# Performance work log

Hardware: AMD Instinct MI355X
Metric: run time of the kernel (lower is better)

The kernel has to match this reference:

```python
import jax, jax.numpy as jnp
import numpy as np

N_NODES = 50000
N_EDGES = 800000
IN_FEAT = 8
H = 128
L = 6
NUM_GRAPHS = 64
EPS_MSG = 1e-7
EPS_SM = 1e-16
LN_EPS = 1e-5


def _ln(x, g, b):
    mu = jnp.mean(x, axis=-1, keepdims=True)
    var = jnp.var(x, axis=-1, keepdims=True)
    return (x - mu) * jax.lax.rsqrt(var + LN_EPS) * g + b


def setup_inputs() -> dict:
    key = jax.random.key(0)
    ks = jax.random.split(key, 12)
    x = jax.random.normal(ks[0], (N_NODES, IN_FEAT), dtype=jnp.float32)
    edge_index = jax.random.randint(ks[1], (2, N_EDGES), 0, N_NODES)
    batch_ids = jnp.sort(jax.random.randint(ks[2], (N_NODES,), 0, NUM_GRAPHS))
    s = 0.05
    return {
        "x": x,
        "edge_index": edge_index,
        "batch_ids": batch_ids,
        "node_W": jax.random.normal(ks[3], (IN_FEAT, H), jnp.float32) * s,
        "node_b": jnp.zeros((H,), jnp.float32),
        "ln_g": jnp.ones((L, H), jnp.float32),
        "ln_b": jnp.zeros((L, H), jnp.float32),
        "t": jnp.ones((L,), jnp.float32),
        "W1": jax.random.normal(ks[4], (L, H, 2 * H), jnp.float32) * s,
        "b1": jnp.zeros((L, 2 * H), jnp.float32),
        "mln_g": jnp.ones((L, 2 * H), jnp.float32),
        "mln_b": jnp.zeros((L, 2 * H), jnp.float32),
        "W2": jax.random.normal(ks[5], (L, 2 * H, H), jnp.float32) * s,
        "b2": jnp.zeros((L, H), jnp.float32),
    }


def reference(x, edge_index, batch_ids, node_W, node_b, ln_g, ln_b, t, W1, b1, mln_g, mln_b, W2, b2):
    src, dst = edge_index[0], edge_index[1]
    n = x.shape[0]
    # node encoder
    x = x @ node_W + node_b  # [N, H]
    for i in range(L):
        # DeepGCNLayer res+: h = relu(LN(x)); x = x + conv(h)
        h = jax.nn.relu(_ln(x, ln_g[i], ln_b[i]))
        # GENConv message: relu(x_j) + eps
        m = jax.nn.relu(h[src]) + EPS_MSG  # [E, H]
        # softmax aggregation over destination segments (temperature t)
        scaled = m * t[i]
        mx = jax.ops.segment_max(scaled, dst, num_segments=n)
        mx = jnp.where(jnp.isfinite(mx), mx, 0.0)
        e = jnp.exp(scaled - mx[dst])
        denom = jax.ops.segment_sum(e, dst, num_segments=n)
        aggr = jax.ops.segment_sum(m * e, dst, num_segments=n) / (denom + EPS_SM)
        # GENConv: out = mlp(aggr + x_r)
        u = aggr + h
        u = u @ W1[i] + b1[i]
        u = jax.nn.relu(_ln(u, mln_g[i], mln_b[i]))
        u = u @ W2[i] + b2[i]
        x = x + u
    # global_add_pool
    return jax.ops.segment_sum(x, batch_ids, num_segments=NUM_GRAPHS)  # [G, H]
```

## Files before the change

### kernel.cpp

```cpp
#include <hip/hip_runtime.h>
#include <hip/hip_bf16.h>
#include <math.h>

#define N_NODES 50000
#define N_EDGES 800000
#define IN_FEAT 8
#define HDIM 128
#define NLAYERS 6
#define NUM_GRAPHS 64
#define EPS_MSG 1e-7f
#define EPS_SM 1e-16f
#define LN_EPS 1e-5f
#define SCAN_NB 49

typedef __attribute__((ext_vector_type(8))) short short8;
typedef __attribute__((ext_vector_type(4))) float floatx4;

__device__ __forceinline__ ushort f2bf(float x) {
    __hip_bfloat16 h = __float2bfloat16(x);
    return *reinterpret_cast<ushort*>(&h);
}
__device__ __forceinline__ float bf2f(ushort u) {
    unsigned int v = ((unsigned int)u) << 16;
    return __uint_as_float(v);
}

__global__ void k_encode_ln(const float* __restrict__ xin, const float* __restrict__ W,
                            const float* __restrict__ bias, const float* __restrict__ g0,
                            const float* __restrict__ b0, float* __restrict__ X,
                            ushort2* __restrict__ Hb) {
    __shared__ float sW[IN_FEAT * HDIM];
    int tid = threadIdx.x;
    int wid = tid >> 6, lane = tid & 63;
    for (int i = tid; i < IN_FEAT * HDIM; i += 256) sW[i] = W[i];
    __syncthreads();
    int n = blockIdx.x * 4 + wid;
    if (n >= N_NODES) return;
    int c0 = 2 * lane, c1 = 2 * lane + 1;
    float a0 = bias[c0], a1 = bias[c1];
#pragma unroll
    for (int f = 0; f < IN_FEAT; ++f) {
        float xf = xin[n * IN_FEAT + f];
        a0 += xf * sW[f * HDIM + c0];
        a1 += xf * sW[f * HDIM + c1];
    }
    float2 xv; xv.x = a0; xv.y = a1;
    *(float2*)(X + (size_t)n * HDIM + c0) = xv;
    float s = a0 + a1, sq = a0 * a0 + a1 * a1;
#pragma unroll
    for (int off = 32; off; off >>= 1) {
        s += __shfl_xor(s, off, 64);
        sq += __shfl_xor(sq, off, 64);
    }
    float mean = s * (1.f / 128.f);
    float var = sq * (1.f / 128.f) - mean * mean;
    float inv = rsqrtf(var + LN_EPS);
    float h0 = (a0 - mean) * inv * g0[c0] + b0[c0];
    float h1 = (a1 - mean) * inv * g0[c1] + b0[c1];
    ushort2 o;
    o.x = f2bf(fmaxf(h0, 0.f));
    o.y = f2bf(fmaxf(h1, 0.f));
    Hb[(size_t)n * 64 + lane] = o;
}

__global__ void k_hist(const int* __restrict__ dst, int* __restrict__ deg) {
    int i = blockIdx.x * blockDim.x + threadIdx.x;
    if (i < N_EDGES) atomicAdd(&deg[dst[i]], 1);
}

__global__ void k_bsum(const int* __restrict__ deg, int* __restrict__ bsum) {
    int i = blockIdx.x * 1024 + threadIdx.x;
    int v = (i < N_NODES) ? deg[i] : 0;
#pragma unroll
    for (int off = 32; off; off >>= 1) v += __shfl_xor(v, off, 64);
    __shared__ int wsum[16];
    int wid = threadIdx.x >> 6;
    if ((threadIdx.x & 63) == 0) wsum[wid] = v;
    __syncthreads();
    if (threadIdx.x < 16) {
        int s = wsum[threadIdx.x];
#pragma unroll
        for (int off = 8; off; off >>= 1) s += __shfl_xor(s, off, 16);
        if (threadIdx.x == 0) bsum[blockIdx.x] = s;
    }
}

__global__ void k_scan_small(int* __restrict__ bsum) {
    int lane = threadIdx.x;
    int orig = (lane < SCAN_NB) ? bsum[lane] : 0;
    int v = orig;
#pragma unroll
    for (int off = 1; off < 64; off <<= 1) {
        int u = __shfl_up(v, off, 64);
        if (lane >= off) v += u;
    }
    if (lane < SCAN_NB) bsum[lane] = v - orig;
}

__global__ void k_scan_final(const int* __restrict__ deg, const int* __restrict__ bsum,
                             int* __restrict__ row_ptr, int* __restrict__ cursor) {
    __shared__ int wsum[16];
    int i = blockIdx.x * 1024 + threadIdx.x;
    int t = threadIdx.x;
    int lane = t & 63, wid = t >> 6;
    int orig = (i < N_NODES) ? deg[i] : 0;
    int v = orig;
#pragma unroll
    for (int off = 1; off < 64; off <<= 1) {
        int u = __shfl_up(v, off, 64);
        if (lane >= off) v += u;
    }
    if (lane == 63) wsum[wid] = v;
    __syncthreads();
    if (t < 16) {
        int s = wsum[t];
#pragma unroll
        for (int off = 1; off < 16; off <<= 1) {
            int u = __shfl_up(s, off, 16);
            if (t >= off) s += u;
        }
        wsum[t] = s;
    }
    __syncthreads();
    int base = bsum[blockIdx.x] + (wid ? wsum[wid - 1] : 0);
    int excl = base + v - orig;
    if (i < N_NODES) {
        row_ptr[i] = excl;
        cursor[i] = excl;
    }
    if (i == 0) row_ptr[N_NODES] = N_EDGES;
}

__global__ void k_scatter(const int* __restrict__ src, const int* __restrict__ dst,
                          int* __restrict__ cursor, int* __restrict__ csr_src) {
    int i = blockIdx.x * blockDim.x + threadIdx.x;
    if (i < N_EDGES) {
        int pos = atomicAdd(&cursor[dst[i]], 1);
        csr_src[pos] = src[i];
    }
}

__global__ void k_prep(const float* __restrict__ W1, const float* __restrict__ W2,
                       ushort* __restrict__ Wp1, ushort* __restrict__ Wp2) {
    int idx = blockIdx.x * 256 + threadIdx.x;
    if (idx < 24576) {
        int lane = idx & 63;
        int frag = idx >> 6;
        int cf = frag & 15, kb = (frag >> 4) & 3, l = frag >> 6;
        const float* Wl = W1 + (size_t)l * 128 * 256;
        ushort* o = Wp1 + (size_t)idx * 8;
        int k0 = kb * 32 + (lane >> 4) * 8;
        int c = cf * 16 + (lane & 15);
#pragma unroll
        for (int j = 0; j < 8; ++j) o[j] = f2bf(Wl[(k0 + j) * 256 + c]);
    } else if (idx < 49152) {
        int i2 = idx - 24576;
        int lane = i2 & 63;
        int frag = i2 >> 6;
        int cf = frag & 7, kb = (frag >> 3) & 7, l = frag >> 6;
        const float* Wl = W2 + (size_t)l * 256 * 128;
        ushort* o = Wp2 + (size_t)i2 * 8;
        int k0 = kb * 32 + (lane >> 4) * 8;
        int c = cf * 16 + (lane & 15);
#pragma unroll
        for (int j = 0; j < 8; ++j) o[j] = f2bf(Wl[(k0 + j) * 128 + c]);
    }
}

__global__ __launch_bounds__(256) void k_aggr(const ushort2* __restrict__ Hh,
                                              const int* __restrict__ row_ptr,
                                              const int* __restrict__ csr,
                                              const float* __restrict__ t_all,
                                              int layer, ushort2* __restrict__ U) {
    __shared__ float part[2][64][4];
    int tid = threadIdx.x;
    int wid = tid >> 6, lane = tid & 63;
    int local = wid >> 1;
    int half = wid & 1;
    int n = blockIdx.x * 2 + local;
    float tt = t_all[layer];
    int beg = row_ptr[n], end = row_ptr[n + 1];
    int cnt = end - beg;
    int mycnt = (cnt - half + 1) >> 1;
    float den0 = 0.f, den1 = 0.f, num0 = 0.f, num1 = 0.f;
    unsigned laneoff = (unsigned)(lane << 2);

    auto proc = [&](ushort2 c) {
        float m0 = bf2f(c.x) + EPS_MSG;
        float m1 = bf2f(c.y) + EPS_MSG;
        float e0 = __expf(m0 * tt);
        float e1 = __expf(m1 * tt);
        den0 += e0; num0 += m0 * e0;
        den1 += e1; num1 += m1 * e1;
    };
    auto LDI = [&](int k) -> ushort2 {
        int kk = (k < mycnt) ? k : mycnt - 1;
        int sidx = csr[beg + half + 2 * kk];
        return *(const ushort2*)((const char*)Hh + (((unsigned)sidx << 8) + laneoff));
    };

    if (mycnt > 0) {
        ushort2 p0 = LDI(0), p1 = LDI(1), p2 = LDI(2), p3 = LDI(3),
                p4 = LDI(4), p5 = LDI(5), p6 = LDI(6), p7 = LDI(7);
        int e = 0;
        while (e + 8 <= mycnt) {
            ushort2 c0 = p0, c1 = p1, c2 = p2, c3 = p3,
                    c4 = p4, c5 = p5, c6 = p6, c7 = p7;
            p0 = LDI(e + 8);  p1 = LDI(e + 9);  p2 = LDI(e + 10); p3 = LDI(e + 11);
            p4 = LDI(e + 12); p5 = LDI(e + 13); p6 = LDI(e + 14); p7 = LDI(e + 15);
            proc(c0); proc(c1); proc(c2); proc(c3);
            proc(c4); proc(c5); proc(c6); proc(c7);
            e += 8;
        }
        int rem = mycnt - e;
        if (rem > 0) proc(p0);
        if (rem > 1) proc(p1);
        if (rem > 2) proc(p2);
        if (rem > 3) proc(p3);
        if (rem > 4) proc(p4);
        if (rem > 5) proc(p5);
        if (rem > 6) proc(p6);
    }

    if (half == 1) {
        part[local][lane][0] = num0;
        part[local][lane][1] = num1;
        part[local][lane][2] = den0;
        part[local][lane][3] = den1;
    }
    __syncthreads();
    if (half == 0) {
        num0 += part[local][lane][0];
        num1 += part[local][lane][1];
        den0 += part[local][lane][2];
        den1 += part[local][lane][3];
        float a0 = num0 / (den0 + EPS_SM);
        float a1 = num1 / (den1 + EPS_SM);
        ushort2 hs = Hh[(size_t)n * 64 + lane];
        ushort2 o;
        o.x = f2bf(a0 + bf2f(hs.x));
        o.y = f2bf(a1 + bf2f(hs.y));
        U[(size_t)n * 64 + lane] = o;
    }
}

__global__ __launch_bounds__(256) void k_mlp_fused(
    const ushort* __restrict__ U, float* __restrict__ X,
    const short8* __restrict__ Wp1, const short8* __restrict__ Wp2,
    const float* __restrict__ b1, const float* __restrict__ mg,
    const float* __restrict__ mb, const float* __restrict__ b2,
    const float* __restrict__ nlg, const float* __restrict__ nlb,
    ushort* __restrict__ HbOut, int writeHb) {
    __shared__ ushort sBuf[64 * 264];
    __shared__ float sStat[4][64][2];
    __shared__ float sMV[64][2];
    int tid = threadIdx.x;
    int w = tid >> 6, lane = tid & 63;
    int g = lane >> 4, c15 = lane & 15;
    int n0 = blockIdx.x * 64;

#pragma unroll
    for (int i = 0; i < 4; ++i) {
        int id = tid + i * 256;
        int row = id >> 4, cc = id & 15;
        int n = n0 + row;
        short8 v = {0, 0, 0, 0, 0, 0, 0, 0};
        if (n < N_NODES) v = *(const short8*)(U + (size_t)n * 128 + cc * 8);
        *(short8*)(sBuf + row * 136 + cc * 8) = v;
    }
    __syncthreads();

    floatx4 acc1[4][4];
#pragma unroll
    for (int rf = 0; rf < 4; ++rf)
#pragma unroll
        for (int cf = 0; cf < 4; ++cf) acc1[rf][cf] = (floatx4){0.f, 0.f, 0.f, 0.f};

#pragma unroll
    for (int kb = 0; kb < 4; ++kb) {
        short8 bfr[4];
#pragma unroll
        for (int cf = 0; cf < 4; ++cf) bfr[cf] = Wp1[(kb * 16 + w * 4 + cf) * 64 + lane];
        short8 af[4];
#pragma unroll
        for (int rf = 0; rf < 4; ++rf)
            af[rf] = *(const short8*)(sBuf + (rf * 16 + c15) * 136 + kb * 32 + g * 8);
#pragma unroll
        for (int rf = 0; rf < 4; ++rf)
#pragma unroll
            for (int cf = 0; cf < 4; ++cf)
                acc1[rf][cf] = __builtin_amdgcn_mfma_f32_16x16x32_bf16(af[rf], bfr[cf], acc1[rf][cf], 0, 0, 0);
    }

    int colb = w * 64;
    float bv[4], gv[4], bbv[4];
#pragma unroll
    for (int cf = 0; cf < 4; ++cf) {
        int c = colb + cf * 16 + c15;
        bv[cf] = b1[c]; gv[cf] = mg[c]; bbv[cf] = mb[c];
    }
    float sS[4][4], sQ[4][4];
#pragma unroll
    for (int rf = 0; rf < 4; ++rf)
#pragma unroll
        for (int reg = 0; reg < 4; ++reg) {
            float s = 0.f, q = 0.f;
#pragma unroll
            for (int cf = 0; cf < 4; ++cf) {
                float v = acc1[rf][cf][reg] + bv[cf];
                acc1[rf][cf][reg] = v;
                s += v; q += v * v;
            }
            sS[rf][reg] = s; sQ[rf][reg] = q;
        }
#pragma unroll
    for (int off = 1; off < 16; off <<= 1)
#pragma unroll
        for (int rf = 0; rf < 4; ++rf)
#pragma unroll
            for (int reg = 0; reg < 4; ++reg) {
                sS[rf][reg] += __shfl_xor(sS[rf][reg], off, 64);
                sQ[rf][reg] += __shfl_xor(sQ[rf][reg], off, 64);
            }
    if (c15 == 0) {
#pragma unroll
        for (int rf = 0; rf < 4; ++rf)
#pragma unroll
            for (int reg = 0; reg < 4; ++reg) {
                int row = rf * 16 + g * 4 + reg;
                sStat[w][row][0] = sS[rf][reg];
                sStat[w][row][1] = sQ[rf][reg];
            }
    }
    __syncthreads();
    if (tid < 64) {
        float s = sStat[0][tid][0] + sStat[1][tid][0] + sStat[2][tid][0] + sStat[3][tid][0];
        float q = sStat[0][tid][1] + sStat[1][tid][1] + sStat[2][tid][1] + sStat[3][tid][1];
        float mean = s * (1.f / 256.f);
        float var = q * (1.f / 256.f) - mean * mean;
        sMV[tid][0] = mean;
        sMV[tid][1] = rsqrtf(var + LN_EPS);
    }
    __syncthreads();

#pragma unroll
    for (int rf = 0; rf < 4; ++rf)
#pragma unroll
        for (int reg = 0; reg < 4; ++reg) {
            int row = rf * 16 + g * 4 + reg;
            float mean = sMV[row][0], inv = sMV[row][1];
#pragma unroll
            for (int cf = 0; cf < 4; ++cf) {
                float v = (acc1[rf][cf][reg] - mean) * inv * gv[cf] + bbv[cf];
                sBuf[row * 264 + colb + cf * 16 + c15] = f2bf(fmaxf(v, 0.f));
            }
        }
    __syncthreads();

    floatx4 acc2[4][2];
#pragma unroll
    for (int rf = 0; rf < 4; ++rf) {
        acc2[rf][0] = (floatx4){0.f, 0.f, 0.f, 0.f};
        acc2[rf][1] = (floatx4){0.f, 0.f, 0.f, 0.f};
    }
#pragma unroll
    for (int kb = 0; kb < 8; ++kb) {
        short8 bfr[2];
#pragma unroll
        for (int cf = 0; cf < 2; ++cf) bfr[cf] = Wp2[(kb * 8 + w * 2 + cf) * 64 + lane];
        short8 af[4];
#pragma unroll
        for (int rf = 0; rf < 4; ++rf)
            af[rf] = *(const short8*)(sBuf + (rf * 16 + c15) * 264 + kb * 32 + g * 8);
#pragma unroll
        for (int rf = 0; rf < 4; ++rf)
#pragma unroll
            for (int cf = 0; cf < 2; ++cf)
                acc2[rf][cf] = __builtin_amdgcn_mfma_f32_16x16x32_bf16(af[rf], bfr[cf], acc2[rf][cf], 0, 0, 0);
    }

    float b2v[2];
    b2v[0] = b2[w * 32 + c15];
    b2v[1] = b2[w * 32 + 16 + c15];
    float gn[2] = {0.f, 0.f}, bn[2] = {0.f, 0.f};
    if (writeHb) {
        gn[0] = nlg[w * 32 + c15];      bn[0] = nlb[w * 32 + c15];
        gn[1] = nlg[w * 32 + 16 + c15]; bn[1] = nlb[w * 32 + 16 + c15];
    }
#pragma unroll
    for (int rf = 0; rf < 4; ++rf)
#pragma unroll
        for (int reg = 0; reg < 4; ++reg) {
            int row = rf * 16 + g * 4 + reg;
            int n = n0 + row;
            float s = 0.f, q = 0.f;
#pragma unroll
            for (int cf = 0; cf < 2; ++cf) {
                float xold = (n < N_NODES) ? X[(size_t)n * 128 + w * 32 + cf * 16 + c15] : 0.f;
                float v = xold + acc2[rf][cf][reg] + b2v[cf];
                acc2[rf][cf][reg] = v;
                s += v; q += v * v;
            }
            if (writeHb) {
#pragma unroll
                for (int off = 1; off < 16; off <<= 1) {
                    s += __shfl_xor(s, off, 64);
                    q += __shfl_xor(q, off, 64);
                }
                if (c15 == 0) {
                    sStat[w][row][0] = s;
                    sStat[w][row][1] = q;
                }
            }
        }
    if (writeHb) {
        __syncthreads();
        if (tid < 64) {
            float s = sStat[0][tid][0] + sStat[1][tid][0] + sStat[2][tid][0] + sStat[3][tid][0];
            float q = sStat[0][tid][1] + sStat[1][tid][1] + sStat[2][tid][1] + sStat[3][tid][1];
            float mean = s * (1.f / 128.f);
            float var = q * (1.f / 128.f) - mean * mean;
            sMV[tid][0] = mean;
            sMV[tid][1] = rsqrtf(var + LN_EPS);
        }
        __syncthreads();
    }
#pragma unroll
    for (int rf = 0; rf < 4; ++rf)
#pragma unroll
        for (int reg = 0; reg < 4; ++reg) {
            int row = rf * 16 + g * 4 + reg;
            int n = n0 + row;
            if (n < N_NODES) {
                float mean = 0.f, inv = 0.f;
                if (writeHb) { mean = sMV[row][0]; inv = sMV[row][1]; }
#pragma unroll
                for (int cf = 0; cf < 2; ++cf) {
                    int col = w * 32 + cf * 16 + c15;
                    float v = acc2[rf][cf][reg];
                    X[(size_t)n * 128 + col] = v;
                    if (writeHb) {
                        float h = (v - mean) * inv * gn[cf] + bn[cf];
                        HbOut[(size_t)n * 128 + col] = f2bf(fmaxf(h, 0.f));
                    }
                }
            }
        }
}

__global__ void k_pool(const float* __restrict__ X, const int* __restrict__ batch,
                       float* __restrict__ out) {
    __shared__ int sBat[128];
    int c = threadIdx.x;
    int n0 = blockIdx.x * 128;
    int nend = n0 + 128; if (nend > N_NODES) nend = N_NODES;
    sBat[c] = (n0 + c < N_NODES) ? batch[n0 + c] : -1;
    __syncthreads();
    float acc = 0.f;
    int cur = sBat[0];
    for (int n = n0; n < nend; ++n) {
        int g = sBat[n - n0];
        if (g != cur) {
            atomicAdd(&out[cur * HDIM + c], acc);
            acc = 0.f;
            cur = g;
        }
        acc += X[(size_t)n * HDIM + c];
    }
    if (nend > n0) atomicAdd(&out[cur * HDIM + c], acc);
}

extern "C" void kernel_launch(void* const* d_in, const int* in_sizes, int n_in,
                              void* d_out, int out_size, void* d_ws, size_t ws_size,
                              hipStream_t stream) {
    const float* x_in   = (const float*)d_in[0];
    const int*   eidx   = (const int*)d_in[1];
    const int*   batch  = (const int*)d_in[2];
    const float* node_W = (const float*)d_in[3];
    const float* node_b = (const float*)d_in[4];
    const float* ln_g   = (const float*)d_in[5];
    const float* ln_b   = (const float*)d_in[6];
    const float* t_all  = (const float*)d_in[7];
    const float* W1     = (const float*)d_in[8];
    const float* b1     = (const float*)d_in[9];
    const float* mg     = (const float*)d_in[10];
    const float* mb     = (const float*)d_in[11];
    const float* W2     = (const float*)d_in[12];
    const float* b2     = (const float*)d_in[13];
    float* out = (float*)d_out;

    char* ws = (char*)d_ws;
    float*  X   = (float*)(ws + 0);
    ushort2* Hb = (ushort2*)(ws + 25600000);
    ushort2* U  = (ushort2*)(ws + 38400000);
    ushort* Wp1 = (ushort*)(ws + 51200000);
    ushort* Wp2 = (ushort*)(ws + 51600000);
    int* deg     = (int*)(ws + 52000000);
    int* row_ptr = (int*)(ws + 52200064);
    int* cursor  = (int*)(ws + 52400128);
    int* csr_src = (int*)(ws + 52600192);
    int* bsum    = (int*)(ws + 55800192);

    const int* e_src = eidx;
    const int* e_dst = eidx + N_EDGES;

    hipMemsetAsync(deg, 0, N_NODES * sizeof(int), stream);
    k_hist<<<(N_EDGES + 255) / 256, 256, 0, stream>>>(e_dst, deg);
    k_bsum<<<SCAN_NB, 1024, 0, stream>>>(deg, bsum);
    k_scan_small<<<1, 64, 0, stream>>>(bsum);
    k_scan_final<<<SCAN_NB, 1024, 0, stream>>>(deg, bsum, row_ptr, cursor);
    k_scatter<<<(N_EDGES + 255) / 256, 256, 0, stream>>>(e_src, e_dst, cursor, csr_src);
    k_prep<<<192, 256, 0, stream>>>(W1, W2, Wp1, Wp2);
    k_encode_ln<<<12500, 256, 0, stream>>>(x_in, node_W, node_b, ln_g, ln_b, X, Hb);

    for (int l = 0; l < NLAYERS; ++l) {
        k_aggr<<<25000, 256, 0, stream>>>(Hb, row_ptr, csr_src, t_all, l, U);
        int wh = (l < NLAYERS - 1) ? 1 : 0;
        const float* nlg = ln_g + (wh ? (l + 1) : 0) * HDIM;
        const float* nlb = ln_b + (wh ? (l + 1) : 0) * HDIM;
        k_mlp_fused<<<(N_NODES + 63) / 64, 256, 0, stream>>>(
            (const ushort*)U, X,
            (const short8*)(Wp1 + (size_t)l * 32768), (const short8*)(Wp2 + (size_t)l * 32768),
            b1 + l * 256, mg + l * 256, mb + l * 256, b2 + l * 128,
            nlg, nlb, (ushort*)Hb, wh);
    }

    hipMemsetAsync(out, 0, NUM_GRAPHS * HDIM * sizeof(float), stream);
    k_pool<<<(N_NODES + 127) / 128, 128, 0, stream>>>(X, batch, out);
}
```

Before: 669.0 us.

## Store node features in FP8, residual stream in bf16, CSR indices as ushort

The gathered node activations move from bf16 to FP8 (e4m3 packed conversion), the residual stream X from fp32 to bf16, and CSR source indices from int32 to 16-bit, which cuts the bytes moved by the gather-heavy aggregation and by the MLP read/write. The softmax exp becomes exp2 with a prescaled temperature, and the prefetch now uses predicated loads instead of clamped indices. Node ids up to 50000 fit in 16 bits. FP8 activations and a bf16 residual accumulated across six layers lose a lot of precision and may fail tolerance checks.

New measurement: 797.9 us. 19.3% more time.

```diff
diff --git a/kernel.cpp b/kernel.cpp
--- a/kernel.cpp
+++ b/kernel.cpp
@@ -15,6 +15,7 @@
 
 typedef __attribute__((ext_vector_type(8))) short short8;
 typedef __attribute__((ext_vector_type(4))) float floatx4;
+typedef __attribute__((ext_vector_type(2))) float floatx2;
 
 __device__ __forceinline__ ushort f2bf(float x) {
     __hip_bfloat16 h = __float2bfloat16(x);
@@ -24,11 +25,18 @@
     unsigned int v = ((unsigned int)u) << 16;
     return __uint_as_float(v);
 }
+__device__ __forceinline__ ushort pk_fp8(float a, float b) {
+    int r = __builtin_amdgcn_cvt_pk_fp8_f32(a, b, 0, false);
+    return (ushort)(r & 0xffff);
+}
+__device__ __forceinline__ floatx2 upk_fp8(ushort v) {
+    return __builtin_amdgcn_cvt_pk_f32_fp8((int)(unsigned)v, false);
+}
 
 __global__ void k_encode_ln(const float* __restrict__ xin, const float* __restrict__ W,
                             const float* __restrict__ bias, const float* __restrict__ g0,
-                            const float* __restrict__ b0, float* __restrict__ X,
-                            ushort2* __restrict__ Hb) {
+                            const float* __restrict__ b0, ushort* __restrict__ X,
+                            ushort* __restrict__ Hb8) {
     __shared__ float sW[IN_FEAT * HDIM];
     int tid = threadIdx.x;
     int wid = tid >> 6, lane = tid & 63;
@@ -44,8 +52,8 @@
         a0 += xf * sW[f * HDIM + c0];
         a1 += xf * sW[f * HDIM + c1];
     }
-    float2 xv; xv.x = a0; xv.y = a1;
-    *(float2*)(X + (size_t)n * HDIM + c0) = xv;
+    ushort2 xv; xv.x = f2bf(a0); xv.y = f2bf(a1);
+    *(ushort2*)(X + (size_t)n * HDIM + c0) = xv;
     float s = a0 + a1, sq = a0 * a0 + a1 * a1;
 #pragma unroll
     for (int off = 32; off; off >>= 1) {
@@ -57,10 +65,7 @@
     float inv = rsqrtf(var + LN_EPS);
     float h0 = (a0 - mean) * inv * g0[c0] + b0[c0];
     float h1 = (a1 - mean) * inv * g0[c1] + b0[c1];
-    ushort2 o;
-    o.x = f2bf(fmaxf(h0, 0.f));
-    o.y = f2bf(fmaxf(h1, 0.f));
-    Hb[(size_t)n * 64 + lane] = o;
+    Hb8[(size_t)n * 64 + lane] = pk_fp8(fmaxf(h0, 0.f), fmaxf(h1, 0.f));
 }
 
 __global__ void k_hist(const int* __restrict__ dst, int* __restrict__ deg) {
@@ -132,11 +137,11 @@
 }
 
 __global__ void k_scatter(const int* __restrict__ src, const int* __restrict__ dst,
-                          int* __restrict__ cursor, int* __restrict__ csr_src) {
+                          int* __restrict__ cursor, ushort* __restrict__ csr_src) {
     int i = blockIdx.x * blockDim.x + threadIdx.x;
     if (i < N_EDGES) {
         int pos = atomicAdd(&cursor[dst[i]], 1);
-        csr_src[pos] = src[i];
+        csr_src[pos] = (ushort)src[i];
     }
 }
 
@@ -167,59 +172,70 @@
     }
 }
 
-__global__ __launch_bounds__(256) void k_aggr(const ushort2* __restrict__ Hh,
+__global__ __launch_bounds__(256) void k_aggr(const ushort* __restrict__ Hb8,
                                               const int* __restrict__ row_ptr,
-                                              const int* __restrict__ csr,
+                                              const ushort* __restrict__ csr,
                                               const float* __restrict__ t_all,
-                                              int layer, ushort2* __restrict__ U) {
+                                              int layer, ushort* __restrict__ U) {
     __shared__ float part[2][64][4];
     int tid = threadIdx.x;
     int wid = tid >> 6, lane = tid & 63;
     int local = wid >> 1;
     int half = wid & 1;
     int n = blockIdx.x * 2 + local;
-    float tt = t_all[layer];
-    int beg = row_ptr[n], end = row_ptr[n + 1];
-    int cnt = end - beg;
+    float ts = t_all[layer] * 1.44269504f;
+    int beg = row_ptr[n], cnt = row_ptr[n + 1] - beg;
     int mycnt = (cnt - half + 1) >> 1;
     float den0 = 0.f, den1 = 0.f, num0 = 0.f, num1 = 0.f;
-    unsigned laneoff = (unsigned)(lane << 2);
-
-    auto proc = [&](ushort2 c) {
-        float m0 = bf2f(c.x) + EPS_MSG;
-        float m1 = bf2f(c.y) + EPS_MSG;
-        float e0 = __expf(m0 * tt);
-        float e1 = __expf(m1 * tt);
-        den0 += e0; num0 += m0 * e0;
-        den1 += e1; num1 += m1 * e1;
+
+    auto RAW = [&](int k) -> ushort {
+        int sidx = (int)csr[beg + half + 2 * k];
+        return *(const ushort*)((const char*)Hb8 + (((unsigned)sidx) << 7) + (unsigned)(lane << 1));
     };
-    auto LDI = [&](int k) -> ushort2 {
-        int kk = (k < mycnt) ? k : mycnt - 1;
-        int sidx = csr[beg + half + 2 * kk];
-        return *(const ushort2*)((const char*)Hh + (((unsigned)sidx << 8) + laneoff));
+    auto proc = [&](ushort v) {
+        floatx2 f = upk_fp8(v);
+        float m0 = f.x + EPS_MSG;
+        float m1 = f.y + EPS_MSG;
+        float e0 = exp2f(m0 * ts);
+        float e1 = exp2f(m1 * ts);
+        den0 += e0; num0 = fmaf(m0, e0, num0);
+        den1 += e1; num1 = fmaf(m1, e1, num1);
     };
 
     if (mycnt > 0) {
-        ushort2 p0 = LDI(0), p1 = LDI(1), p2 = LDI(2), p3 = LDI(3),
-                p4 = LDI(4), p5 = LDI(5), p6 = LDI(6), p7 = LDI(7);
-        int e = 0;
-        while (e + 8 <= mycnt) {
-            ushort2 c0 = p0, c1 = p1, c2 = p2, c3 = p3,
-                    c4 = p4, c5 = p5, c6 = p6, c7 = p7;
-            p0 = LDI(e + 8);  p1 = LDI(e + 9);  p2 = LDI(e + 10); p3 = LDI(e + 11);
-            p4 = LDI(e + 12); p5 = LDI(e + 13); p6 = LDI(e + 14); p7 = LDI(e + 15);
+        ushort q0 = 0, q1 = 0, q2 = 0, q3 = 0, q4 = 0, q5 = 0, q6 = 0, q7 = 0;
+        q0 = RAW(0);
+        if (mycnt > 1) q1 = RAW(1);
+        if (mycnt > 2) q2 = RAW(2);
+        if (mycnt > 3) q3 = RAW(3);
+        if (mycnt > 4) q4 = RAW(4);
+        if (mycnt > 5) q5 = RAW(5);
+        if (mycnt > 6) q6 = RAW(6);
+        if (mycnt > 7) q7 = RAW(7);
+        int p = 0;
+        while (p + 8 <= mycnt) {
+            ushort c0 = q0, c1 = q1, c2 = q2, c3 = q3,
+                   c4 = q4, c5 = q5, c6 = q6, c7 = q7;
+            if (p + 8 < mycnt)  q0 = RAW(p + 8);
+            if (p + 9 < mycnt)  q1 = RAW(p + 9);
+            if (p + 10 < mycnt) q2 = RAW(p + 10);
+            if (p + 11 < mycnt) q3 = RAW(p + 11);
+            if (p + 12 < mycnt) q4 = RAW(p + 12);
+            if (p + 13 < mycnt) q5 = RAW(p + 13);
+            if (p + 14 < mycnt) q6 = RAW(p + 14);
+            if (p + 15 < mycnt) q7 = RAW(p + 15);
             proc(c0); proc(c1); proc(c2); proc(c3);
             proc(c4); proc(c5); proc(c6); proc(c7);
-            e += 8;
-        }
-        int rem = mycnt - e;
-        if (rem > 0) proc(p0);
-        if (rem > 1) proc(p1);
-        if (rem > 2) proc(p2);
-        if (rem > 3) proc(p3);
-        if (rem > 4) proc(p4);
-        if (rem > 5) proc(p5);
-        if (rem > 6) proc(p6);
+            p += 8;
+        }
+        int rem = mycnt - p;
+        if (rem > 0) proc(q0);
+        if (rem > 1) proc(q1);
+        if (rem > 2) proc(q2);
+        if (rem > 3) proc(q3);
+        if (rem > 4) proc(q4);
+        if (rem > 5) proc(q5);
+        if (rem > 6) proc(q6);
     }
 
     if (half == 1) {
@@ -234,23 +250,21 @@
         num1 += part[local][lane][1];
         den0 += part[local][lane][2];
         den1 += part[local][lane][3];
-        float a0 = num0 / (den0 + EPS_SM);
-        float a1 = num1 / (den1 + EPS_SM);
-        ushort2 hs = Hh[(size_t)n * 64 + lane];
+        floatx2 hs = upk_fp8(*(const ushort*)((const char*)Hb8 + (((unsigned)n) << 7) + (unsigned)(lane << 1)));
         ushort2 o;
-        o.x = f2bf(a0 + bf2f(hs.x));
-        o.y = f2bf(a1 + bf2f(hs.y));
-        U[(size_t)n * 64 + lane] = o;
+        o.x = f2bf(num0 / (den0 + EPS_SM) + hs.x);
+        o.y = f2bf(num1 / (den1 + EPS_SM) + hs.y);
+        *(ushort2*)(U + (size_t)n * 128 + 2 * lane) = o;
     }
 }
 
 __global__ __launch_bounds__(256) void k_mlp_fused(
-    const ushort* __restrict__ U, float* __restrict__ X,
+    const ushort* __restrict__ U, ushort* __restrict__ X,
     const short8* __restrict__ Wp1, const short8* __restrict__ Wp2,
     const float* __restrict__ b1, const float* __restrict__ mg,
     const float* __restrict__ mb, const float* __restrict__ b2,
     const float* __restrict__ nlg, const float* __restrict__ nlb,
-    ushort* __restrict__ HbOut, int writeHb) {
+    unsigned char* __restrict__ Hb8Out, int writeHb) {
     __shared__ ushort sBuf[64 * 264];
     __shared__ float sStat[4][64][2];
     __shared__ float sMV[64][2];
@@ -396,7 +410,7 @@
             float s = 0.f, q = 0.f;
 #pragma unroll
             for (int cf = 0; cf < 2; ++cf) {
-                float xold = (n < N_NODES) ? X[(size_t)n * 128 + w * 32 + cf * 16 + c15] : 0.f;
+                float xold = (n < N_NODES) ? bf2f(X[(size_t)n * 128 + w * 32 + cf * 16 + c15]) : 0.f;
                 float v = xold + acc2[rf][cf][reg] + b2v[cf];
                 acc2[rf][cf][reg] = v;
                 s += v; q += v * v;
@@ -438,17 +452,18 @@
                 for (int cf = 0; cf < 2; ++cf) {
                     int col = w * 32 + cf * 16 + c15;
                     float v = acc2[rf][cf][reg];
-                    X[(size_t)n * 128 + col] = v;
+                    X[(size_t)n * 128 + col] = f2bf(v);
                     if (writeHb) {
-                        float h = (v - mean) * inv * gn[cf] + bn[cf];
-                        HbOut[(size_t)n * 128 + col] = f2bf(fmaxf(h, 0.f));
+                        float h = fmaxf((v - mean) * inv * gn[cf] + bn[cf], 0.f);
+                        int pk = __builtin_amdgcn_cvt_pk_fp8_f32(h, h, 0, false);
+                        Hb8Out[(size_t)n * 128 + col] = (unsigned char)(pk & 0xff);
                     }
                 }
             }
         }
 }
 
-__global__ void k_pool(const float* __restrict__ X, const int* __restrict__ batch,
+__global__ void k_pool(const ushort* __restrict__ X, const int* __restrict__ batch,
                        float* __restrict__ out) {
     __shared__ int sBat[128];
     int c = threadIdx.x;
@@ -465,7 +480,7 @@
             acc = 0.f;
             cur = g;
         }
-        acc += X[(size_t)n * HDIM + c];
+        acc += bf2f(X[(size_t)n * HDIM + c]);
     }
     if (nend > n0) atomicAdd(&out[cur * HDIM + c], acc);
 }
@@ -490,16 +505,16 @@
     float* out = (float*)d_out;
 
     char* ws = (char*)d_ws;
-    float*  X   = (float*)(ws + 0);
-    ushort2* Hb = (ushort2*)(ws + 25600000);
-    ushort2* U  = (ushort2*)(ws + 38400000);
-    ushort* Wp1 = (ushort*)(ws + 51200000);
-    ushort* Wp2 = (ushort*)(ws + 51600000);
-    int* deg     = (int*)(ws + 52000000);
-    int* row_ptr = (int*)(ws + 52200064);
-    int* cursor  = (int*)(ws + 52400128);
-    int* csr_src = (int*)(ws + 52600192);
-    int* bsum    = (int*)(ws + 55800192);
+    ushort* X    = (ushort*)(ws + 0);
+    ushort* Hb8  = (ushort*)(ws + 12800000);
+    ushort* U    = (ushort*)(ws + 19200000);
+    ushort* Wp1  = (ushort*)(ws + 32000000);
+    ushort* Wp2  = (ushort*)(ws + 32400000);
+    int* deg     = (int*)(ws + 32800000);
+    int* row_ptr = (int*)(ws + 33000064);
+    int* cursor  = (int*)(ws + 33200128);
+    ushort* csr_src = (ushort*)(ws + 33400192);
+    int* bsum    = (int*)(ws + 35000192);
 
     const int* e_src = eidx;
     const int* e_dst = eidx + N_EDGES;
@@ -511,18 +526,18 @@
     k_scan_final<<<SCAN_NB, 1024, 0, stream>>>(deg, bsum, row_ptr, cursor);
     k_scatter<<<(N_EDGES + 255) / 256, 256, 0, stream>>>(e_src, e_dst, cursor, csr_src);
     k_prep<<<192, 256, 0, stream>>>(W1, W2, Wp1, Wp2);
-    k_encode_ln<<<12500, 256, 0, stream>>>(x_in, node_W, node_b, ln_g, ln_b, X, Hb);
+    k_encode_ln<<<12500, 256, 0, stream>>>(x_in, node_W, node_b, ln_g, ln_b, X, Hb8);
 
     for (int l = 0; l < NLAYERS; ++l) {
-        k_aggr<<<25000, 256, 0, stream>>>(Hb, row_ptr, csr_src, t_all, l, U);
+        k_aggr<<<25000, 256, 0, stream>>>(Hb8, row_ptr, csr_src, t_all, l, U);
         int wh = (l < NLAYERS - 1) ? 1 : 0;
         const float* nlg = ln_g + (wh ? (l + 1) : 0) * HDIM;
         const float* nlb = ln_b + (wh ? (l + 1) : 0) * HDIM;
         k_mlp_fused<<<(N_NODES + 63) / 64, 256, 0, stream>>>(
-            (const ushort*)U, X,
+            U, X,
             (const short8*)(Wp1 + (size_t)l * 32768), (const short8*)(Wp2 + (size_t)l * 32768),
             b1 + l * 256, mg + l * 256, mb + l * 256, b2 + l * 128,
-            nlg, nlb, (ushort*)Hb, wh);
+            nlg, nlb, (unsigned char*)Hb8, wh);
     }
 
     hipMemsetAsync(out, 0, NUM_GRAPHS * HDIM * sizeof(float), stream);
```
